# Optimization experiments

Hardware: AMD Instinct MI355X
Metric: run time of the kernel (lower is better)

## Reference

```python
import jax, jax.numpy as jnp
import numpy as np

H = 16  # heads
EPS_LN = 1e-5

def _ln(x, g, b):
    m = jnp.mean(x, axis=-1, keepdims=True)
    v = jnp.mean((x - m) ** 2, axis=-1, keepdims=True)
    return (x - m) / jnp.sqrt(v + EPS_LN) * g + b

def setup_inputs() -> dict:
    key = jax.random.key(0)
    B, L, d, mlp = 4, 4096, 1024, 4096
    ks = jax.random.split(key, 12)
    s = 0.02
    inp = {
        'x':   jax.random.normal(ks[0], (B, L, d), jnp.float32),
        'Wq':  jax.random.normal(ks[1], (d, d), jnp.float32) * s,
        'bq':  jnp.zeros((d,), jnp.float32),
        'gq':  jnp.ones((d,), jnp.float32),
        'betaq': jnp.zeros((d,), jnp.float32),
        'Wk':  jax.random.normal(ks[2], (d, d), jnp.float32) * s,
        'bk':  jnp.zeros((d,), jnp.float32),
        'gk':  jnp.ones((d,), jnp.float32),
        'betak': jnp.zeros((d,), jnp.float32),
        'Wv':  jax.random.normal(ks[3], (d, d), jnp.float32) * s,
        'bv':  jnp.zeros((d,), jnp.float32),
        'gv':  jnp.ones((d,), jnp.float32),
        'betav': jnp.zeros((d,), jnp.float32),
        'Wfq': jax.random.normal(ks[4], (d, d), jnp.float32) * s,
        'bfq': jnp.zeros((d,), jnp.float32),
        'Wfk': jax.random.normal(ks[5], (d, d), jnp.float32) * s,
        'bfk': jnp.zeros((d,), jnp.float32),
        'ga':  jnp.ones((d,), jnp.float32),
        'ba':  jnp.zeros((d,), jnp.float32),
        'W1':  jax.random.normal(ks[6], (d, mlp), jnp.float32) * s,
        'b1':  jnp.zeros((mlp,), jnp.float32),
        'W2':  jax.random.normal(ks[7], (mlp, d), jnp.float32) * s,
        'b2':  jnp.zeros((d,), jnp.float32),
    }
    return inp

def _fwd(x, Wq, bq, gq, betaq, Wk, bk, gk, betak, Wv, bv, gv, betav,
         Wfq, bfq, Wfk, bfk, ga, ba, W1, b1, W2, b2):
    B, L, d = x.shape
    D = d // H
    # Q/K/V projections + LayerNorm (dropout is eval-mode identity)
    Q = _ln(x @ Wq + bq, gq, betaq)                      # [B,L,d]
    Kc = _ln(x @ Wk + bk, gk, betak)                     # [B,L,d]
    Vc = _ln(x @ Wv + bv, gv, betav)                     # [B,L,d]
    # prepend zero token to K and V (add_zero_token=True)
    z = jnp.zeros((B, 1, d), x.dtype)
    K = jnp.concatenate([z, Kc], axis=1)                 # [B,Lk,d], Lk=L+1
    V = jnp.concatenate([z, Vc], axis=1)
    # kernel feature maps: tanh(Linear(.)) + 1
    phi_Q = jnp.tanh(Q @ Wfq + bfq) + 1.0
    phi_K = jnp.tanh(K @ Wfk + bfk) + 1.0
    split = lambda t: t.reshape(B, t.shape[1], H, D).transpose(0, 2, 1, 3)
    Qh, Kh, Vh = split(Q), split(K), split(V)            # [B,H,L(,k),D]
    pQ, pK = split(phi_Q), split(phi_K)
    # probe-softmax gating of phi_K
    q_probe = jnp.mean(Qh, axis=2) / jnp.sqrt(jnp.asarray(D, x.dtype))  # [B,H,D]
    score = jax.nn.softmax(jnp.einsum('bhd,bhkd->bhk', q_probe, Kh), axis=-1)  # [B,H,Lk]
    pKw = pK * score[..., None]                          # [B,H,Lk,D]
    # linear-attention fast path
    KV = jnp.einsum('bhkd,bhke->bhde', pKw, Vh)          # [B,H,D,D]
    Ksum = jnp.sum(pKw, axis=2)                          # [B,H,D]
    num = jnp.einsum('bhqd,bhde->bhqe', pQ, KV)          # [B,H,L,D]
    den = jnp.einsum('bhqd,bhd->bhq', pQ, Ksum)[..., None] + 1e-6
    out = num / den                                      # [B,H,L,D]
    out = out.transpose(0, 2, 1, 3).reshape(B, L, d)     # merge heads
    a = _ln(out, ga, ba)                                 # attn_norm
    # Residual MLP: a + Linear2(GELU(Linear1(a)))  (exact erf GELU)
    h = a + (jax.nn.gelu(a @ W1 + b1, approximate=False) @ W2 + b2)
    return h + x                                         # outer residual

def reference(x, Wq, bq, gq, betaq, Wk, bk, gk, betak, Wv, bv, gv, betav,
              Wfq, bfq, Wfk, bfk, ga, ba, W1, b1, W2, b2):
    return _fwd(x, Wq, bq, gq, betaq, Wk, bk, gk, betak, Wv, bv, gv, betav,
                Wfq, bfq, Wfk, bfk, ga, ba, W1, b1, W2, b2)
```

## Files before the change

### kernel.cpp

```cpp
#include <hip/hip_runtime.h>
#include <cstddef>
#include <cstdint>

static constexpr int Bc   = 4;
static constexpr int Lq   = 4096;
static constexpr int Dm   = 1024;
static constexpr int Dmlp = 4096;
static constexpr int Mrows = Bc * Lq;
static constexpr int Lk1   = Lq + 1;

typedef unsigned short u16;
typedef __bf16 bf16_t;
typedef bf16_t bf16x8 __attribute__((ext_vector_type(8)));
typedef float  f32x4  __attribute__((ext_vector_type(4)));

__device__ __forceinline__ u16 f2b(float f) {
    uint32_t u = __builtin_bit_cast(uint32_t, f);
    return (u16)((u + 0x7FFFu + ((u >> 16) & 1u)) >> 16);
}
__device__ __forceinline__ float b2f(u16 h) {
    uint32_t u = ((uint32_t)h) << 16;
    return __builtin_bit_cast(float, u);
}

#define GLL16(gsrc, ldst) \
    __builtin_amdgcn_global_load_lds( \
        (const __attribute__((address_space(1))) void*)(gsrc), \
        (__attribute__((address_space(3))) void*)(ldst), 16, 0, 0)

__global__ __launch_bounds__(256)
void zero_kernel(float* __restrict__ p, int n) {
    const int i = blockIdx.x * 256 + threadIdx.x;
    if (i < n) p[i] = 0.0f;
}

__global__ __launch_bounds__(256)
void cvt_bf16_kernel(const float* __restrict__ in, u16* __restrict__ outp, int n) {
    for (int i = (blockIdx.x * 256 + threadIdx.x) * 4; i < n; i += gridDim.x * 256 * 4) {
        float4 v = *(const float4*)&in[i];
        ushort4 o = { f2b(v.x), f2b(v.y), f2b(v.z), f2b(v.w) };
        *(ushort4*)&outp[i] = o;
    }
}

__global__ __launch_bounds__(256)
void transpose_bf16_kernel(const float* __restrict__ in, u16* __restrict__ outp,
                           int R, int C) {
    __shared__ float tile[64][65];
    const int r0 = blockIdx.y * 64, c0 = blockIdx.x * 64;
    const int t = threadIdx.x;
    const int lr = t >> 2, lc0 = (t & 3) * 16;
    #pragma unroll
    for (int j = 0; j < 4; ++j) {
        float4 v = *(const float4*)&in[(size_t)(r0 + lr) * C + c0 + lc0 + j * 4];
        tile[lr][lc0 + j * 4 + 0] = v.x;
        tile[lr][lc0 + j * 4 + 1] = v.y;
        tile[lr][lc0 + j * 4 + 2] = v.z;
        tile[lr][lc0 + j * 4 + 3] = v.w;
    }
    __syncthreads();
    const int oc = t >> 2, rr0 = (t & 3) * 16;
    union { u16 u[16]; uint4 v[2]; } pk;
    #pragma unroll
    for (int j = 0; j < 16; ++j) pk.u[j] = f2b(tile[rr0 + j][oc]);
    u16* po = &outp[(size_t)(c0 + oc) * R + r0 + rr0];
    *(uint4*)&po[0] = pk.v[0];
    *(uint4*)&po[8] = pk.v[1];
}

template<int ACT, bool RES, bool ACCUM, bool BIAS, bool OBF16>
__global__ __launch_bounds__(512, 1)
void mfma_gemm256(const u16* __restrict__ A, int ldA,
                  const u16* __restrict__ Bt, int ldB,
                  const float* __restrict__ bias,
                  void* __restrict__ Cout,
                  const u16* __restrict__ res1, const float* __restrict__ res2,
                  int M, int N, int K) {
    __shared__ u16 ldsA[4][8192];
    __shared__ u16 ldsB[4][8192];
    const int tid = threadIdx.x;
    const int l   = tid & 63;
    const int w   = tid >> 6;
    const int wm  = w >> 2;
    const int wn  = w & 3;
    const int l16 = l & 15, l4 = l >> 4;

    const int gx = N >> 8;
    int bid = blockIdx.x;
    bid = (bid & 7) * ((int)gridDim.x >> 3) + (bid >> 3);
    const int brow = (bid / gx) << 8;
    const int bcol = (bid % gx) << 8;

    const int srow = w * 16 + (l >> 2);
    const int skof = ((l & 3) ^ ((l >> 3) & 3)) << 3;
    const u16* gA = A  + (size_t)(brow + srow) * ldA + skof;
    const u16* gB = Bt + (size_t)(bcol + srow) * ldB + skof;
    const size_t gsA = (size_t)128 * ldA;
    const size_t gsB = (size_t)128 * ldB;
    const int ldst = w * 512 + l * 8;

    const int koff_rd = ((l4 ^ ((l16 >> 1) & 3)) << 3);
    const int aRdBase = (wm * 128 + l16) * 32 + koff_rd;
    const int bRdBase = (wn * 64  + l16) * 32 + koff_rd;

    f32x4 acc[8][4];
    const f32x4 zf = {0.f, 0.f, 0.f, 0.f};
    #pragma unroll
    for (int m = 0; m < 8; ++m)
        #pragma unroll
        for (int n = 0; n < 4; ++n) acc[m][n] = zf;

    auto stageA = [&](int slot, int kelem) {
        const u16* s = gA + (size_t)kelem;
        GLL16(s,       &ldsA[slot][ldst]);
        GLL16(s + gsA, &ldsA[slot][ldst + 4096]);
    };
    auto stageB = [&](int slot, int kelem) {
        const u16* s = gB + (size_t)kelem;
        GLL16(s,       &ldsB[slot][ldst]);
        GLL16(s + gsB, &ldsB[slot][ldst + 4096]);
    };

    const int T = K >> 5;
    stageA(0, 0);  stageB(0, 0);
    stageA(1, 32); stageB(1, 32);
    stageA(2, 64); stageB(2, 64);

    auto step = [&](int t, int waitsel, bool do_stage) {
        asm volatile("s_waitcnt lgkmcnt(0)" ::: "memory");
        if (waitsel == 0)      asm volatile("s_waitcnt vmcnt(8)" ::: "memory");
        else if (waitsel == 1) asm volatile("s_waitcnt vmcnt(4)" ::: "memory");
        else                   asm volatile("s_waitcnt vmcnt(0)" ::: "memory");
        asm volatile("s_barrier" ::: "memory");
        const int slot = t & 3;
        bf16x8 afr[4], bfr[4];
        #pragma unroll
        for (int n = 0; n < 4; ++n)
            bfr[n] = *(const bf16x8*)&ldsB[slot][bRdBase + n * 512];
        #pragma unroll
        for (int m = 0; m < 4; ++m)
            afr[m] = *(const bf16x8*)&ldsA[slot][aRdBase + m * 512];
        if (do_stage) stageA((t + 3) & 3, (t + 3) * 32);
        __builtin_amdgcn_s_setprio(1);
        #pragma unroll
        for (int m = 0; m < 4; ++m)
            #pragma unroll
            for (int n = 0; n < 4; ++n)
                acc[m][n] = __builtin_amdgcn_mfma_f32_16x16x32_bf16(
                    afr[m], bfr[n], acc[m][n], 0, 0, 0);
        __builtin_amdgcn_s_setprio(0);
        #pragma unroll
        for (int m = 0; m < 4; ++m)
            afr[m] = *(const bf16x8*)&ldsA[slot][aRdBase + (m + 4) * 512];
        if (do_stage) stageB((t + 3) & 3, (t + 3) * 32);
        __builtin_amdgcn_s_setprio(1);
        #pragma unroll
        for (int m = 0; m < 4; ++m)
            #pragma unroll
            for (int n = 0; n < 4; ++n)
                acc[m + 4][n] = __builtin_amdgcn_mfma_f32_16x16x32_bf16(
                    afr[m], bfr[n], acc[m + 4][n], 0, 0, 0);
        __builtin_amdgcn_s_setprio(0);
    };

    for (int t = 0; t < T - 2; ++t) step(t, 0, (t + 3) < T);
    step(T - 2, 1, false);
    step(T - 1, 2, false);

    float bvn[4];
    int coln[4];
    #pragma unroll
    for (int n = 0; n < 4; ++n) {
        coln[n] = bcol + wn * 64 + n * 16 + l16;
        bvn[n] = BIAS ? bias[coln[n]] : 0.f;
    }
    #pragma unroll
    for (int m = 0; m < 8; ++m) {
        #pragma unroll
        for (int q = 0; q < 4; ++q) {
            const size_t row = (size_t)brow + wm * 128 + m * 16 + l4 * 4 + q;
            #pragma unroll
            for (int n = 0; n < 4; ++n) {
                float v = acc[m][n][q] + bvn[n];
                if (ACT == 1) v = tanhf(v) + 1.0f;
                if (ACT == 2) v = 0.5f * v * (1.0f + erff(v * 0.70710678118654752f));
                const size_t idx = row * (size_t)N + coln[n];
                if (OBF16) {
                    ((u16*)Cout)[idx] = f2b(v);
                } else {
                    float* Cf = (float*)Cout;
                    if (ACCUM) v += Cf[idx];
                    if (RES)   v += b2f(res1[idx]) + res2[idx];
                    Cf[idx] = v;
                }
            }
        }
    }
}

__global__ __launch_bounds__(256)
void ln1024_bf16_kernel(const u16* __restrict__ in, u16* __restrict__ outp,
                        const float* __restrict__ g, const float* __restrict__ be) {
    const size_t base = (size_t)blockIdx.x * Dm;
    const int tid = threadIdx.x;
    ushort4 raw = *(const ushort4*)&in[base + tid * 4];
    float v0 = b2f(raw.x), v1 = b2f(raw.y), v2 = b2f(raw.z), v3 = b2f(raw.w);
    float s  = v0 + v1 + v2 + v3;
    float sq = v0 * v0 + v1 * v1 + v2 * v2 + v3 * v3;
    #pragma unroll
    for (int off = 32; off > 0; off >>= 1) {
        s  += __shfl_down(s,  off, 64);
        sq += __shfl_down(sq, off, 64);
    }
    __shared__ float rs[4], rq[4];
    const int lane = tid & 63, wv = tid >> 6;
    if (lane == 0) { rs[wv] = s; rq[wv] = sq; }
    __syncthreads();
    s  = rs[0] + rs[1] + rs[2] + rs[3];
    sq = rq[0] + rq[1] + rq[2] + rq[3];
    const float mean = s * (1.0f / 1024.0f);
    const float var  = sq * (1.0f / 1024.0f) - mean * mean;
    const float inv  = rsqrtf(var + 1e-5f);
    float4 gv = *(const float4*)&g[tid * 4];
    float4 bv = *(const float4*)&be[tid * 4];
    ushort4 o;
    o.x = f2b((v0 - mean) * inv * gv.x + bv.x);
    o.y = f2b((v1 - mean) * inv * gv.y + bv.y);
    o.z = f2b((v2 - mean) * inv * gv.z + bv.z);
    o.w = f2b((v3 - mean) * inv * gv.w + bv.w);
    *(ushort4*)&outp[base + tid * 4] = o;
}

__global__ __launch_bounds__(256)
void qprobe_kernel(const u16* __restrict__ Q, float* __restrict__ qp) {
    const int b = blockIdx.z;
    const int col = blockIdx.x * 256 + threadIdx.x;
    const int lchunk = Lq / 16;
    const int l0 = blockIdx.y * lchunk;
    const u16* p = Q + ((size_t)b * Lq + l0) * Dm + col;
    float s = 0.f;
    for (int l = 0; l < lchunk; ++l, p += Dm) s += b2f(*p);
    atomicAdd(&qp[b * Dm + col], s * (1.0f / (4096.0f * 8.0f)));
}

__global__ __launch_bounds__(256)
void logits_kernel(const u16* __restrict__ Kc, const float* __restrict__ qp,
                   float* __restrict__ score) {
    const int bh = blockIdx.y, b = bh >> 4, h = bh & 15;
    __shared__ float q[64];
    if (threadIdx.x < 64) q[threadIdx.x] = qp[b * Dm + h * 64 + threadIdx.x];
    __syncthreads();
    const int kr = blockIdx.x * 256 + threadIdx.x;
    const ushort4* krp = (const ushort4*)&Kc[((size_t)b * Lq + kr) * Dm + h * 64];
    float s = 0.f;
    #pragma unroll
    for (int i = 0; i < 16; ++i) {
        ushort4 v = krp[i];
        s += q[i * 4 + 0] * b2f(v.x) + q[i * 4 + 1] * b2f(v.y)
           + q[i * 4 + 2] * b2f(v.z) + q[i * 4 + 3] * b2f(v.w);
    }
    score[(size_t)bh * Lk1 + kr + 1] = s;
    if (blockIdx.x == 0 && threadIdx.x == 0) score[(size_t)bh * Lk1] = 0.f;
}

__global__ __launch_bounds__(256)
void softmax4097_kernel(float* __restrict__ sc) {
    __shared__ float buf[Lk1];
    __shared__ float red[8];
    const size_t base = (size_t)blockIdx.x * Lk1;
    const int tid = threadIdx.x;
    float mx = -1e30f;
    for (int i = tid; i < Lk1; i += 256) { float v = sc[base + i]; buf[i] = v; mx = fmaxf(mx, v); }
    #pragma unroll
    for (int off = 32; off > 0; off >>= 1) mx = fmaxf(mx, __shfl_down(mx, off, 64));
    const int lane = tid & 63, wv = tid >> 6;
    if (lane == 0) red[wv] = mx;
    __syncthreads();
    mx = fmaxf(fmaxf(red[0], red[1]), fmaxf(red[2], red[3]));
    float sum = 0.f;
    for (int i = tid; i < Lk1; i += 256) { float e = expf(buf[i] - mx); buf[i] = e; sum += e; }
    #pragma unroll
    for (int off = 32; off > 0; off >>= 1) sum += __shfl_down(sum, off, 64);
    if (lane == 0) red[4 + wv] = sum;
    __syncthreads();
    sum = red[4] + red[5] + red[6] + red[7];
    const float inv = 1.0f / sum;
    for (int i = tid; i < Lk1; i += 256) sc[base + i] = buf[i] * inv;
}

__global__ __launch_bounds__(256)
void kv_kernel(const u16* __restrict__ phiK, const u16* __restrict__ Vc,
               const float* __restrict__ sc, float* __restrict__ KV) {
    const int bh = blockIdx.y, b = bh >> 4, h = bh & 15;
    const int lchunk = Lq / 8;
    const int l0 = blockIdx.x * lchunk;
    __shared__ float pk[8][64];
    __shared__ float vv[8][64];
    const int i0 = (threadIdx.x >> 4) << 2;
    const int j0 = (threadIdx.x & 15) << 2;
    float acc[4][4] = {};
    for (int lb = l0; lb < l0 + lchunk; lb += 8) {
        #pragma unroll
        for (int q = 0; q < 2; ++q) {
            const int idx = threadIdx.x + q * 256;
            const int r = idx >> 6, c = idx & 63;
            const float scv = sc[(size_t)bh * Lk1 + lb + r + 1];
            const size_t off = ((size_t)b * Lq + lb + r) * Dm + h * 64 + c;
            pk[r][c] = b2f(phiK[off]) * scv;
            vv[r][c] = b2f(Vc[off]);
        }
        __syncthreads();
        #pragma unroll
        for (int r = 0; r < 8; ++r) {
            float ra[4], rb[4];
            #pragma unroll
            for (int i = 0; i < 4; ++i) ra[i] = pk[r][i0 + i];
            #pragma unroll
            for (int j = 0; j < 4; ++j) rb[j] = vv[r][j0 + j];
            #pragma unroll
            for (int i = 0; i < 4; ++i)
                #pragma unroll
                for (int j = 0; j < 4; ++j)
                    acc[i][j] = fmaf(ra[i], rb[j], acc[i][j]);
        }
        __syncthreads();
    }
    #pragma unroll
    for (int i = 0; i < 4; ++i)
        #pragma unroll
        for (int j = 0; j < 4; ++j)
            atomicAdd(&KV[((size_t)bh * 64 + i0 + i) * 64 + j0 + j], acc[i][j]);
}

__global__ __launch_bounds__(64)
void ksum_kernel(const u16* __restrict__ phiK, const float* __restrict__ sc,
                 const float* __restrict__ bfk, float* __restrict__ Ksum) {
    const int bh = blockIdx.y, b = bh >> 4, h = bh & 15;
    const int lchunk = Lq / 8;
    const int l0 = blockIdx.x * lchunk;
    const int dd = threadIdx.x;
    float s = 0.f;
    const u16* pp = &phiK[((size_t)b * Lq + l0) * Dm + h * 64 + dd];
    const float* sp = &sc[(size_t)bh * Lk1 + l0 + 1];
    for (int l = 0; l < lchunk; ++l, pp += Dm) s = fmaf(b2f(*pp), sp[l], s);
    if (blockIdx.x == 0) s += sc[(size_t)bh * Lk1] * (tanhf(bfk[h * 64 + dd]) + 1.0f);
    atomicAdd(&Ksum[bh * 64 + dd], s);
}

__global__ __launch_bounds__(256)
void attnout_kernel(const u16* __restrict__ phiQ, const float* __restrict__ KV,
                    const float* __restrict__ Ksum, u16* __restrict__ outp) {
    const int bh = blockIdx.y, b = bh >> 4, h = bh & 15;
    const int l0 = blockIdx.x * 64;
    __shared__ float kvs[64][64];
    __shared__ float pqs[64][65];
    __shared__ float kss[64];
    __shared__ float dns[64];
    const int tid = threadIdx.x;
    {
        const float* kvg = &KV[(size_t)bh * 4096];
        float* kf = &kvs[0][0];
        #pragma unroll
        for (int j = 0; j < 4; ++j)
            *(float4*)&kf[tid * 16 + j * 4] = *(const float4*)&kvg[tid * 16 + j * 4];
    }
    if (tid < 64) kss[tid] = Ksum[bh * 64 + tid];
    {
        const int row = tid >> 2, c0 = (tid & 3) * 16;
        const u16* pg = &phiQ[((size_t)(b * Lq + l0 + row)) * Dm + h * 64 + c0];
        #pragma unroll
        for (int j = 0; j < 4; ++j) {
            ushort4 u = *(const ushort4*)&pg[j * 4];
            pqs[row][c0 + j * 4 + 0] = b2f(u.x);
            pqs[row][c0 + j * 4 + 1] = b2f(u.y);
            pqs[row][c0 + j * 4 + 2] = b2f(u.z);
            pqs[row][c0 + j * 4 + 3] = b2f(u.w);
        }
    }
    __syncthreads();
    if (tid < 64) {
        float s = 0.f;
        #pragma unroll
        for (int d = 0; d < 64; ++d) s = fmaf(pqs[tid][d], kss[d], s);
        dns[tid] = 1.0f / (s + 1e-6f);
    }
    __syncthreads();
    const int e = tid & 63;
    const int rg = tid >> 6;
    #pragma unroll 2
    for (int p = 0; p < 16; ++p) {
        const int row = p * 4 + rg;
        float acc = 0.f;
        #pragma unroll
        for (int d = 0; d < 64; ++d)
            acc = fmaf(pqs[row][d], kvs[d][e], acc);
        outp[(((size_t)(b * Lq + l0 + row)) << 10) + h * 64 + e] = f2b(acc * dns[row]);
    }
}

extern "C" void kernel_launch(void* const* d_in, const int* in_sizes, int n_in,
                              void* d_out, int out_size, void* d_ws, size_t ws_size,
                              hipStream_t stream) {
    const float* x     = (const float*)d_in[0];
    const float* Wq    = (const float*)d_in[1];
    const float* bq    = (const float*)d_in[2];
    const float* gq    = (const float*)d_in[3];
    const float* betaq = (const float*)d_in[4];
    const float* Wk    = (const float*)d_in[5];
    const float* bk    = (const float*)d_in[6];
    const float* gk    = (const float*)d_in[7];
    const float* betak = (const float*)d_in[8];
    const float* Wv    = (const float*)d_in[9];
    const float* bv    = (const float*)d_in[10];
    const float* gv    = (const float*)d_in[11];
    const float* betav = (const float*)d_in[12];
    const float* Wfq   = (const float*)d_in[13];
    const float* bfq   = (const float*)d_in[14];
    const float* Wfk   = (const float*)d_in[15];
    const float* bfk   = (const float*)d_in[16];
    const float* ga    = (const float*)d_in[17];
    const float* ba    = (const float*)d_in[18];
    const float* W1    = (const float*)d_in[19];
    const float* b1    = (const float*)d_in[20];
    const float* W2    = (const float*)d_in[21];
    const float* b2    = (const float*)d_in[22];
    float* outp = (float*)d_out;

    uint8_t* wsb = (uint8_t*)d_ws;
    size_t off = 0;
    auto alloc = [&](size_t bytes) { void* p = wsb + off; off += bytes; return p; };
    const size_t Md = (size_t)Mrows * Dm;
    u16* B0   = (u16*)alloc(Md * 2);
    u16* B1   = (u16*)alloc(Md * 2);
    u16* B2   = (u16*)alloc(Md * 2);
    u16* Wtq  = (u16*)alloc((size_t)Dm * Dm * 2);
    u16* Wtk  = (u16*)alloc((size_t)Dm * Dm * 2);
    u16* Wtv  = (u16*)alloc((size_t)Dm * Dm * 2);
    u16* Wtfq = (u16*)alloc((size_t)Dm * Dm * 2);
    u16* Wtfk = (u16*)alloc((size_t)Dm * Dm * 2);
    u16* Wt1  = (u16*)alloc((size_t)Dm * Dmlp * 2);
    u16* Wt2  = (u16*)alloc((size_t)Dm * Dmlp * 2);
    float* qp    = (float*)alloc(4096 * 4);
    float* KV    = (float*)alloc((size_t)64 * 64 * 64 * 4);
    float* Ksum  = (float*)alloc(4096 * 4);
    float* score = (float*)alloc((size_t)64 * Lk1 * 4);
    u16* PK = (u16*)outp;
    u16* PQ = (u16*)outp + Md;

    const dim3 blk(256);
    const dim3 blk512(512);
    const dim3 gA(256);
    const dim3 gM(512);

    cvt_bf16_kernel<<<2048, blk, 0, stream>>>(x, B0, (int)Md);
    transpose_bf16_kernel<<<dim3(16, 16), blk, 0, stream>>>(Wq,  Wtq,  Dm, Dm);
    transpose_bf16_kernel<<<dim3(16, 16), blk, 0, stream>>>(Wk,  Wtk,  Dm, Dm);
    transpose_bf16_kernel<<<dim3(16, 16), blk, 0, stream>>>(Wv,  Wtv,  Dm, Dm);
    transpose_bf16_kernel<<<dim3(16, 16), blk, 0, stream>>>(Wfq, Wtfq, Dm, Dm);
    transpose_bf16_kernel<<<dim3(16, 16), blk, 0, stream>>>(Wfk, Wtfk, Dm, Dm);
    transpose_bf16_kernel<<<dim3(64, 16), blk, 0, stream>>>(W1,  Wt1,  Dm, Dmlp);
    transpose_bf16_kernel<<<dim3(16, 64), blk, 0, stream>>>(W2,  Wt2,  Dmlp, Dm);
    {
        const int nz = 4096 + 64 * 64 * 64 + 4096;
        zero_kernel<<<(nz + 255) / 256, blk, 0, stream>>>(qp, nz);
    }

    mfma_gemm256<0, false, false, true, true><<<gA, blk512, 0, stream>>>(
        B0, Dm, Wtq, Dm, bq, B1, nullptr, nullptr, Mrows, Dm, Dm);
    ln1024_bf16_kernel<<<Mrows, blk, 0, stream>>>(B1, B1, gq, betaq);
    mfma_gemm256<0, false, false, true, true><<<gA, blk512, 0, stream>>>(
        B0, Dm, Wtk, Dm, bk, B2, nullptr, nullptr, Mrows, Dm, Dm);
    ln1024_bf16_kernel<<<Mrows, blk, 0, stream>>>(B2, B2, gk, betak);

    qprobe_kernel<<<dim3(Dm / 256, 16, Bc), blk, 0, stream>>>(B1, qp);
    logits_kernel<<<dim3(Lq / 256, 64), blk, 0, stream>>>(B2, qp, score);
    softmax4097_kernel<<<64, blk, 0, stream>>>(score);

    mfma_gemm256<1, false, false, true, true><<<gA, blk512, 0, stream>>>(
        B2, Dm, Wtfk, Dm, bfk, PK, nullptr, nullptr, Mrows, Dm, Dm);
    mfma_gemm256<1, false, false, true, true><<<gA, blk512, 0, stream>>>(
        B1, Dm, Wtfq, Dm, bfq, PQ, nullptr, nullptr, Mrows, Dm, Dm);

    mfma_gemm256<0, false, false, true, true><<<gA, blk512, 0, stream>>>(
        B0, Dm, Wtv, Dm, bv, B1, nullptr, nullptr, Mrows, Dm, Dm);
    ln1024_bf16_kernel<<<Mrows, blk, 0, stream>>>(B1, B1, gv, betav);

    kv_kernel<<<dim3(8, 64), blk, 0, stream>>>(PK, B1, score, KV);
    ksum_kernel<<<dim3(8, 64), dim3(64), 0, stream>>>(PK, score, bfk, Ksum);

    attnout_kernel<<<dim3(Lq / 64, 64), blk, 0, stream>>>(PQ, KV, Ksum, B2);
    ln1024_bf16_kernel<<<Mrows, blk, 0, stream>>>(B2, B2, ga, ba);

    u16* H1 = B0;
    for (int c = 0; c < 2; ++c) {
        mfma_gemm256<2, false, false, true, true><<<gM, blk512, 0, stream>>>(
            B2, Dm, Wt1 + (size_t)c * 2048 * Dm, Dm, b1 + c * 2048,
            H1, nullptr, nullptr, Mrows, 2048, Dm);
        if (c == 0) {
            mfma_gemm256<0, false, false, true, false><<<gA, blk512, 0, stream>>>(
                H1, 2048, Wt2 + (size_t)c * 2048, Dmlp, b2,
                outp, nullptr, nullptr, Mrows, Dm, 2048);
        } else {
            mfma_gemm256<0, true, true, false, false><<<gA, blk512, 0, stream>>>(
                H1, 2048, Wt2 + (size_t)c * 2048, Dmlp, nullptr,
                outp, B2, x, Mrows, Dm, 2048);
        }
    }
}
```

Baseline: 876.2 us.

## Move attention output product to bf16 MFMA with transposed bf16 KV

Replaces the scalar-FMA attention output kernel with an MFMA-based kernel that processes 256 query rows per block. The fp32 KV state is first transposed and converted to bf16 so it can be held in registers as B fragments. phiQ is staged through swizzled LDS via direct global-to-LDS loads. The goal is to cut the FMA-bound cost of the L×D×D product, at the price of an extra small kernel and bf16 rounding of KV.

```diff
diff --git a/kernel.cpp b/kernel.cpp
--- a/kernel.cpp
+++ b/kernel.cpp
@@ -64,6 +64,31 @@
     #pragma unroll
     for (int j = 0; j < 16; ++j) pk.u[j] = f2b(tile[rr0 + j][oc]);
     u16* po = &outp[(size_t)(c0 + oc) * R + r0 + rr0];
+    *(uint4*)&po[0] = pk.v[0];
+    *(uint4*)&po[8] = pk.v[1];
+}
+
+__global__ __launch_bounds__(256)
+void kvt_cvt_kernel(const float* __restrict__ KV, u16* __restrict__ KVT) {
+    const int bh = blockIdx.x;
+    __shared__ float t[64][65];
+    const int tid = threadIdx.x;
+    const int r = tid >> 2, c0 = (tid & 3) * 16;
+    const float* src = &KV[(size_t)bh * 4096];
+    #pragma unroll
+    for (int j = 0; j < 4; ++j) {
+        float4 v = *(const float4*)&src[r * 64 + c0 + j * 4];
+        t[r][c0 + j * 4 + 0] = v.x;
+        t[r][c0 + j * 4 + 1] = v.y;
+        t[r][c0 + j * 4 + 2] = v.z;
+        t[r][c0 + j * 4 + 3] = v.w;
+    }
+    __syncthreads();
+    const int e = tid >> 2, d0 = (tid & 3) * 16;
+    union { u16 u[16]; uint4 v[2]; } pk;
+    #pragma unroll
+    for (int j = 0; j < 16; ++j) pk.u[j] = f2b(t[d0 + j][e]);
+    u16* po = &KVT[(size_t)bh * 4096 + e * 64 + d0];
     *(uint4*)&po[0] = pk.v[0];
     *(uint4*)&po[8] = pk.v[1];
 }
@@ -347,54 +372,88 @@
     atomicAdd(&Ksum[bh * 64 + dd], s);
 }
 
-__global__ __launch_bounds__(256)
-void attnout_kernel(const u16* __restrict__ phiQ, const float* __restrict__ KV,
-                    const float* __restrict__ Ksum, u16* __restrict__ outp) {
+__global__ __launch_bounds__(256, 2)
+void attnout_mfma_kernel(const u16* __restrict__ phiQ, const u16* __restrict__ KVT,
+                         const float* __restrict__ Ksum, u16* __restrict__ outp) {
+    __shared__ u16 pqs[256 * 64];
+    __shared__ float kss[64];
+    __shared__ float dns[256];
     const int bh = blockIdx.y, b = bh >> 4, h = bh & 15;
-    const int l0 = blockIdx.x * 64;
-    __shared__ float kvs[64][64];
-    __shared__ float pqs[64][65];
-    __shared__ float kss[64];
-    __shared__ float dns[64];
+    const int l0 = blockIdx.x * 256;
     const int tid = threadIdx.x;
+    const int l = tid & 63, w = tid >> 6;
+    const int l16 = l & 15, l4 = l >> 4;
+
+    bf16x8 bfr[4][2];
     {
-        const float* kvg = &KV[(size_t)bh * 4096];
-        float* kf = &kvs[0][0];
-        #pragma unroll
-        for (int j = 0; j < 4; ++j)
-            *(float4*)&kf[tid * 16 + j * 4] = *(const float4*)&kvg[tid * 16 + j * 4];
+        const u16* kb = KVT + (size_t)bh * 4096;
+        #pragma unroll
+        for (int n = 0; n < 4; ++n)
+            #pragma unroll
+            for (int kk = 0; kk < 2; ++kk)
+                bfr[n][kk] = *(const bf16x8*)&kb[(n * 16 + l16) * 64 + kk * 32 + l4 * 8];
     }
     if (tid < 64) kss[tid] = Ksum[bh * 64 + tid];
+
     {
-        const int row = tid >> 2, c0 = (tid & 3) * 16;
-        const u16* pg = &phiQ[((size_t)(b * Lq + l0 + row)) * Dm + h * 64 + c0];
-        #pragma unroll
-        for (int j = 0; j < 4; ++j) {
-            ushort4 u = *(const ushort4*)&pg[j * 4];
-            pqs[row][c0 + j * 4 + 0] = b2f(u.x);
-            pqs[row][c0 + j * 4 + 1] = b2f(u.y);
-            pqs[row][c0 + j * 4 + 2] = b2f(u.z);
-            pqs[row][c0 + j * 4 + 3] = b2f(u.w);
-        }
-    }
-    __syncthreads();
-    if (tid < 64) {
+        const int rsub = tid >> 3;
+        const int ssrc = ((tid & 7) ^ (rsub & 7)) * 8;
+        u16* ldst = &pqs[(size_t)tid * 8];
+        #pragma unroll
+        for (int j = 0; j < 8; ++j) {
+            const u16* g = phiQ + (((size_t)(b * Lq + l0 + j * 32 + rsub)) << 10)
+                          + h * 64 + ssrc;
+            GLL16(g, ldst + j * 2048);
+        }
+    }
+    __syncthreads();
+
+    {
+        const int r7 = tid & 7;
         float s = 0.f;
         #pragma unroll
-        for (int d = 0; d < 64; ++d) s = fmaf(pqs[tid][d], kss[d], s);
+        for (int sl = 0; sl < 8; ++sl) {
+            bf16x8 v = *(const bf16x8*)&pqs[tid * 64 + ((sl ^ r7) << 3)];
+            #pragma unroll
+            for (int j = 0; j < 8; ++j) s = fmaf(b2f(((u16*)&v)[j]), kss[sl * 8 + j], s);
+        }
         dns[tid] = 1.0f / (s + 1e-6f);
     }
-    __syncthreads();
-    const int e = tid & 63;
-    const int rg = tid >> 6;
-    #pragma unroll 2
-    for (int p = 0; p < 16; ++p) {
-        const int row = p * 4 + rg;
-        float acc = 0.f;
-        #pragma unroll
-        for (int d = 0; d < 64; ++d)
-            acc = fmaf(pqs[row][d], kvs[d][e], acc);
-        outp[(((size_t)(b * Lq + l0 + row)) << 10) + h * 64 + e] = f2b(acc * dns[row]);
+
+    f32x4 acc[4][4];
+    const f32x4 zf = {0.f, 0.f, 0.f, 0.f};
+    #pragma unroll
+    for (int m = 0; m < 4; ++m)
+        #pragma unroll
+        for (int n = 0; n < 4; ++n) acc[m][n] = zf;
+    #pragma unroll
+    for (int kk = 0; kk < 2; ++kk) {
+        bf16x8 afr[4];
+        #pragma unroll
+        for (int m = 0; m < 4; ++m) {
+            const int row = w * 64 + m * 16 + l16;
+            afr[m] = *(const bf16x8*)&pqs[row * 64 + (((kk * 4 + l4) ^ (row & 7)) << 3)];
+        }
+        #pragma unroll
+        for (int m = 0; m < 4; ++m)
+            #pragma unroll
+            for (int n = 0; n < 4; ++n)
+                acc[m][n] = __builtin_amdgcn_mfma_f32_16x16x32_bf16(
+                    afr[m], bfr[n][kk], acc[m][n], 0, 0, 0);
+    }
+    __syncthreads();
+
+    #pragma unroll
+    for (int m = 0; m < 4; ++m) {
+        #pragma unroll
+        for (int q = 0; q < 4; ++q) {
+            const int rl = w * 64 + m * 16 + l4 * 4 + q;
+            const float dn = dns[rl];
+            const size_t rowg = ((size_t)(b * Lq + l0 + rl)) << 10;
+            #pragma unroll
+            for (int n = 0; n < 4; ++n)
+                outp[rowg + h * 64 + n * 16 + l16] = f2b(acc[m][n][q] * dn);
+        }
     }
 }
 
@@ -444,6 +503,7 @@
     float* KV    = (float*)alloc((size_t)64 * 64 * 64 * 4);
     float* Ksum  = (float*)alloc(4096 * 4);
     float* score = (float*)alloc((size_t)64 * Lk1 * 4);
+    u16* KVT     = (u16*)alloc((size_t)64 * 64 * 64 * 2);
     u16* PK = (u16*)outp;
     u16* PQ = (u16*)outp + Md;
 
@@ -487,8 +547,9 @@
 
     kv_kernel<<<dim3(8, 64), blk, 0, stream>>>(PK, B1, score, KV);
     ksum_kernel<<<dim3(8, 64), dim3(64), 0, stream>>>(PK, score, bfk, Ksum);
-
-    attnout_kernel<<<dim3(Lq / 64, 64), blk, 0, stream>>>(PQ, KV, Ksum, B2);
+    kvt_cvt_kernel<<<64, blk, 0, stream>>>(KV, KVT);
+
+    attnout_mfma_kernel<<<dim3(Lq / 256, 64), blk, 0, stream>>>(PQ, KVT, Ksum, B2);
     ln1024_bf16_kernel<<<Mrows, blk, 0, stream>>>(B2, B2, ga, ba);
 
     u16* H1 = B0;
```

Measured after the change: 782.5 us, median of 2. -10.7%, faster.
